# Performance work log

Measured on AMD Instinct MI355X. Metric: run time of the kernel, lower is better.

Reference implementation:

```python
import jax, jax.numpy as jnp
import numpy as np

# spconv.SparseConv4d(C_in, 16, (1,3,3,3), stride=1, padding=0) on spatial_shape [1000,1000,40]:
# leading kernel dim is size 1, so this is a regular (non-submanifold) 3D sparse conv,
# valid padding -> output spatial shape (998, 998, 38). Implemented as gather-GEMM-scatter:
# input point p contributes feat(p) @ W[k] to output coord p - offset[k] for each of 27 taps.

N = 200000
C_IN = 64
C_OUT = 16
K = 3
OUT_SP = (998, 998, 38)  # 1000-3+1, 1000-3+1, 40-3+1
SENT = OUT_SP[0] * OUT_SP[1] * OUT_SP[2]  # sentinel linear index for invalid taps


def setup_inputs() -> dict:
    key = jax.random.key(0)
    k1, k2, k3, k4, k5, k6 = jax.random.split(key, 6)
    feats = jax.random.normal(k1, (N, C_IN), dtype=jnp.float32)
    x = jax.random.randint(k2, (N,), 0, 1000, dtype=jnp.int32)
    y = jax.random.randint(k3, (N,), 0, 1000, dtype=jnp.int32)
    z = jax.random.randint(k4, (N,), 0, 40, dtype=jnp.int32)
    coords = jnp.stack([jnp.zeros((N,), jnp.int32), x, y, z], axis=1)  # [N,4] (b,x,y,z)
    fan_in = C_IN * K * K * K
    W = jax.random.normal(k5, (K * K * K, C_IN, C_OUT), dtype=jnp.float32) / np.sqrt(fan_in)
    bias = jax.random.normal(k6, (C_OUT,), dtype=jnp.float32) * 0.01
    return {"input": feats, "coords": coords, "W": W, "bias": bias}


def reference(input, coords, W, bias):
    # kernel tap offsets, C-order over (kx,ky,kz) in [0,3)^3 -> [27,3]
    off = jnp.stack(
        jnp.meshgrid(jnp.arange(K), jnp.arange(K), jnp.arange(K), indexing="ij"),
        axis=-1,
    ).reshape(K * K * K, 3).astype(jnp.int32)
    xyz = coords[:, 1:4]                              # [N,3]
    oc = xyz[:, None, :] - off[None, :, :]            # [N,27,3] output coord per tap
    out_sp = jnp.array(OUT_SP, dtype=jnp.int32)
    valid = jnp.all((oc >= 0) & (oc < out_sp), axis=-1)  # [N,27]
    lin = oc[..., 0] * (OUT_SP[1] * OUT_SP[2]) + oc[..., 1] * OUT_SP[2] + oc[..., 2]
    lin = jnp.where(valid, lin, SENT).reshape(-1)     # [N*27]

    # gather-GEMM: per-tap GEMM over all active voxels
    contrib = jnp.einsum("nc,kco->nko", input, W)     # [N,27,16]
    contrib = jnp.where(valid[..., None], contrib, 0.0).reshape(-1, C_OUT)

    NK = N * (K * K * K)
    uniq, inv = jnp.unique(lin, return_inverse=True, size=NK, fill_value=SENT)
    inv = inv.reshape(-1)
    # scatter-add into unique output sites
    out = jax.ops.segment_sum(contrib, inv, num_segments=NK)  # [NK,16]
    cnt = jax.ops.segment_sum(valid.reshape(-1).astype(jnp.int32), inv, num_segments=NK)
    out = out + jnp.where(cnt[:, None] > 0, bias[None, :], 0.0)
    return out, uniq
```

## Files before the change

kernel.cpp:

```cpp
#include <hip/hip_runtime.h>

#define N_PTS   200000
#define CIN     64
#define COUT    16
#define KK      27
#define SXD     998
#define SYD     998
#define SZD     38
#define STRX    (SYD*SZD)
#define SENTV   (SXD*SYD*SZD)
#define NKTOT   (N_PTS*KK)
#define NWORDS  ((SENTV+31)/32)
#define NCHUNK  ((NWORDS+255)/256)

typedef float f32x4 __attribute__((ext_vector_type(4)));

__global__ void mark_kernel(const int* __restrict__ coords, unsigned* __restrict__ bitmap,
                            unsigned* __restrict__ multi) {
    int n = blockIdx.x * blockDim.x + threadIdx.x;
    if (n >= N_PTS) return;
    int4 c = ((const int4*)coords)[n];
    int x = c.y, y = c.z, z = c.w;
    int zlo = z - 2; if (zlo < 0) zlo = 0;
    int zhi = z;     if (zhi > SZD - 1) zhi = SZD - 1;
    unsigned nb = (unsigned)(zhi - zlo + 1);
    unsigned mseed = (1u << nb) - 1u;
    #pragma unroll
    for (int dx = 0; dx < 3; dx++) {
        int ox = x - dx;
        if (ox < 0 || ox >= SXD) continue;
        #pragma unroll
        for (int dy = 0; dy < 3; dy++) {
            int oy = y - dy;
            if (oy < 0 || oy >= SYD) continue;
            int lin = ox*STRX + oy*SZD + zlo;
            unsigned w = (unsigned)lin >> 5;
            unsigned b = (unsigned)lin & 31u;
            unsigned lowm = mseed << b;
            unsigned old = atomicOr(&bitmap[w], lowm);
            unsigned col = old & lowm;
            if (col) atomicOr(&multi[w], col);
            if (b + nb > 32u) {
                unsigned highm = mseed >> (32u - b);
                unsigned old2 = atomicOr(&bitmap[w+1], highm);
                unsigned col2 = old2 & highm;
                if (col2) atomicOr(&multi[w+1], col2);
            }
        }
    }
}

__global__ void chunk_sums_kernel(const unsigned* __restrict__ bitmap, unsigned* __restrict__ csums) {
    int w = blockIdx.x * 256 + threadIdx.x;
    unsigned c = (w < NWORDS) ? (unsigned)__popc(bitmap[w]) : 0u;
    __shared__ unsigned s[256];
    s[threadIdx.x] = c;
    __syncthreads();
    for (int off = 128; off > 0; off >>= 1) {
        if (threadIdx.x < off) s[threadIdx.x] += s[threadIdx.x + off];
        __syncthreads();
    }
    if (threadIdx.x == 0) csums[blockIdx.x] = s[0];
}

__global__ void scan_chunks_kernel(const unsigned* __restrict__ csums,
                                   unsigned* __restrict__ cprefix,
                                   unsigned* __restrict__ Uptr) {
    __shared__ unsigned s[256];
    __shared__ unsigned run_s;
    if (threadIdx.x == 0) run_s = 0;
    __syncthreads();
    for (int base = 0; base < NCHUNK; base += 256) {
        int i = base + threadIdx.x;
        unsigned v = (i < NCHUNK) ? csums[i] : 0u;
        s[threadIdx.x] = v;
        __syncthreads();
        for (int off = 1; off < 256; off <<= 1) {
            unsigned t = (threadIdx.x >= off) ? s[threadIdx.x - off] : 0u;
            __syncthreads();
            s[threadIdx.x] += t;
            __syncthreads();
        }
        unsigned run = run_s;
        if (i < NCHUNK) cprefix[i] = run + s[threadIdx.x] - v;
        unsigned tile_total = s[255];
        __syncthreads();
        if (threadIdx.x == 255) run_s = run + tile_total;
        __syncthreads();
    }
    if (threadIdx.x == 0) Uptr[0] = run_s;
}

__global__ void word_prefix_kernel(const unsigned* __restrict__ bitmap,
                                   const unsigned* __restrict__ cprefix,
                                   unsigned* __restrict__ wprefix) {
    int w = blockIdx.x * 256 + threadIdx.x;
    unsigned v = (w < NWORDS) ? (unsigned)__popc(bitmap[w]) : 0u;
    __shared__ unsigned s[256];
    s[threadIdx.x] = v;
    __syncthreads();
    for (int off = 1; off < 256; off <<= 1) {
        unsigned t = (threadIdx.x >= off) ? s[threadIdx.x - off] : 0u;
        __syncthreads();
        s[threadIdx.x] += t;
        __syncthreads();
    }
    if (w < NWORDS) wprefix[w] = cprefix[blockIdx.x] + s[threadIdx.x] - v;
}

__global__ void fill_out_kernel(float* __restrict__ out, const float* __restrict__ bias,
                                const unsigned* __restrict__ Uptr) {
    unsigned U = Uptr[0];
    unsigned i = blockIdx.x * blockDim.x + threadIdx.x;
    if (i >= (unsigned)NKTOT * 4u) return;
    unsigned row = i >> 2;
    int q = i & 3;
    float4 v;
    if (row < U) v = ((const float4*)bias)[q];
    else         v = make_float4(0.f, 0.f, 0.f, 0.f);
    ((float4*)out)[i] = v;
}

__global__ void fill_uniq_kernel(float* __restrict__ uniq) {
    unsigned i = blockIdx.x * blockDim.x + threadIdx.x;
    if (i < (unsigned)NKTOT) uniq[i] = (float)SENTV;
}

__global__ void tail_kernel(float* __restrict__ out, float* __restrict__ uniq,
                            const unsigned* __restrict__ Uptr) {
    unsigned U = Uptr[0];
    unsigned i = blockIdx.x * blockDim.x + threadIdx.x;
    if (i >= (unsigned)NKTOT || i < U) return;
    f32x4 z4 = {0.f, 0.f, 0.f, 0.f};
    f32x4* dst = (f32x4*)(out + (size_t)i * COUT);
    #pragma unroll
    for (int q = 0; q < 4; q++) __builtin_nontemporal_store(z4, dst + q);
    __builtin_nontemporal_store((float)SENTV, uniq + i);
}

__global__ void write_uniq_kernel(const unsigned* __restrict__ bitmap,
                                  const unsigned* __restrict__ multi,
                                  const unsigned* __restrict__ wprefix,
                                  float* __restrict__ uniq,
                                  float* __restrict__ out,
                                  const float* __restrict__ bias,
                                  int do_bias) {
    int w = blockIdx.x * 256 + threadIdx.x;
    if (w >= NWORDS) return;
    unsigned bits = bitmap[w];
    if (!bits) return;
    unsigned mbits = do_bias ? multi[w] : 0u;
    f32x4 bv[4];
    #pragma unroll
    for (int q = 0; q < 4; q++) bv[q] = ((const f32x4*)bias)[q];
    unsigned r = wprefix[w];
    while (bits) {
        int b = __ffs(bits) - 1;
        bits &= bits - 1;
        uniq[r] = (float)(w * 32 + b);
        if ((mbits >> b) & 1u) {
            f32x4* dst = (f32x4*)(out + (size_t)r * COUT);
            #pragma unroll
            for (int q = 0; q < 4; q++) __builtin_nontemporal_store(bv[q], dst + q);
        }
        r++;
    }
}

__launch_bounds__(64)
__global__ void scatter_mm_kernel(const float* __restrict__ feats,
                                  const int* __restrict__ coords,
                                  const float* __restrict__ W,
                                  const float* __restrict__ bias,
                                  const unsigned* __restrict__ bitmap,
                                  const unsigned* __restrict__ multi,
                                  const unsigned* __restrict__ wprefix,
                                  float* __restrict__ out) {
    int n = blockIdx.x * 64 + threadIdx.x;
    if (n >= N_PTS) return;
    int4 cc = ((const int4*)coords)[n];
    int x = cc.y, y = cc.z, z = cc.w;

    f32x4 f[CIN/4];
    const f32x4* fin4 = (const f32x4*)(feats + (size_t)n * CIN);
    #pragma unroll
    for (int i = 0; i < CIN/4; i++) f[i] = __builtin_nontemporal_load(fin4 + i);

    f32x4 bv[4];
    #pragma unroll
    for (int q = 0; q < 4; q++) bv[q] = ((const f32x4*)bias)[q];

    #pragma unroll 1
    for (int m = 0; m < KK; m++) {
        int ox = x - (m/9), oy = y - ((m/3)%3), oz = z - (m%3);
        if (ox < 0 || ox >= SXD || oy < 0 || oy >= SYD || oz < 0 || oz >= SZD) continue;
        int lin = ox*STRX + oy*SZD + oz;
        unsigned word = (unsigned)lin >> 5, bit = (unsigned)lin & 31u;
        unsigned rank = wprefix[word] + (unsigned)__popc(bitmap[word] & ((1u << bit) - 1u));
        bool is_multi = (multi[word] >> bit) & 1u;

        const float* wk = W + (size_t)m * CIN * COUT;
        float acc[COUT];
        #pragma unroll
        for (int o = 0; o < COUT; o++) acc[o] = 0.f;
        #pragma unroll
        for (int c4 = 0; c4 < CIN/4; c4++) {
            f32x4 fv = f[c4];
            const float* wrow = wk + c4 * 4 * COUT;
            #pragma unroll
            for (int o = 0; o < COUT; o++) {
                acc[o] += fv.x * wrow[o] + fv.y * wrow[COUT + o]
                        + fv.z * wrow[2*COUT + o] + fv.w * wrow[3*COUT + o];
            }
        }

        float* dst = out + (size_t)rank * COUT;
        if (!is_multi) {
            #pragma unroll
            for (int q = 0; q < 4; q++) {
                f32x4 v;
                v.x = acc[q*4+0] + bv[q].x;
                v.y = acc[q*4+1] + bv[q].y;
                v.z = acc[q*4+2] + bv[q].z;
                v.w = acc[q*4+3] + bv[q].w;
                __builtin_nontemporal_store(v, ((f32x4*)dst) + q);
            }
        } else {
            #pragma unroll
            for (int o = 0; o < COUT; o++) atomicAdd(dst + o, acc[o]);
        }
    }
}

extern "C" void kernel_launch(void* const* d_in, const int* in_sizes, int n_in,
                              void* d_out, int out_size, void* d_ws, size_t ws_size,
                              hipStream_t stream) {
    const float* feats  = (const float*)d_in[0];
    const int*   coords = (const int*)d_in[1];
    const float* W      = (const float*)d_in[2];
    const float* bias   = (const float*)d_in[3];
    float* out  = (float*)d_out;
    float* uniq = out + (size_t)NKTOT * COUT;

    unsigned* ws      = (unsigned*)d_ws;
    unsigned* bitmap  = ws;
    unsigned* multi   = ws + NWORDS;
    unsigned* wprefix = ws + 2 * (size_t)NWORDS;
    unsigned* csums   = ws + 3 * (size_t)NWORDS;
    unsigned* cprefix = csums + NCHUNK;
    unsigned* Uptr    = cprefix + NCHUNK;

    size_t needed = ((size_t)3 * NWORDS + 2 * NCHUNK + 1) * sizeof(unsigned);
    bool have_multi = ws_size >= needed;
    if (!have_multi) {
        multi   = bitmap;
        wprefix = ws + NWORDS;
        csums   = ws + 2 * (size_t)NWORDS;
        cprefix = csums + NCHUNK;
        Uptr    = cprefix + NCHUNK;
        hipMemsetAsync(bitmap, 0, (size_t)NWORDS * sizeof(unsigned), stream);
    } else {
        hipMemsetAsync(bitmap, 0, 2 * (size_t)NWORDS * sizeof(unsigned), stream);
    }

    mark_kernel<<<(N_PTS + 255) / 256, 256, 0, stream>>>(coords, bitmap, multi);
    chunk_sums_kernel<<<NCHUNK, 256, 0, stream>>>(bitmap, csums);
    scan_chunks_kernel<<<1, 256, 0, stream>>>(csums, cprefix, Uptr);
    word_prefix_kernel<<<NCHUNK, 256, 0, stream>>>(bitmap, cprefix, wprefix);

    if (have_multi) {
        write_uniq_kernel<<<NCHUNK, 256, 0, stream>>>(bitmap, multi, wprefix, uniq, out, bias, 1);
        tail_kernel<<<(NKTOT + 255) / 256, 256, 0, stream>>>(out, uniq, Uptr);
    } else {
        fill_out_kernel<<<(NKTOT * 4 + 255) / 256, 256, 0, stream>>>(out, bias, Uptr);
        fill_uniq_kernel<<<(NKTOT + 255) / 256, 256, 0, stream>>>(uniq);
        write_uniq_kernel<<<NCHUNK, 256, 0, stream>>>(bitmap, multi, wprefix, uniq, out, bias, 0);
    }

    scatter_mm_kernel<<<(N_PTS + 63) / 64, 64, 0, stream>>>(
        feats, coords, W, bias, bitmap, multi, wprefix, out);
}
```

Baseline: 1.253 ms.

## Interleave bitmap metadata, bucket-sort points spatially, and stage uniq writes in LDS

Bitmap, multi-mask and word prefix are interleaved into one 16-byte record per word, so the scatter kernel needs a single uint4 load per tap instead of three scattered loads. Points are bucket-sorted by coarse (x/8, y/8) tiles using a histogram, an exclusive scan and an atomic placement pass. Neighbouring threads therefore touch nearby bitmap words and output rows. write_uniq now gathers each block's unique indices in shared memory and writes them out coalesced, in exchange for extra passes, more workspace and an 8192-float shared buffer per block.

```diff
diff --git a/kernel.cpp b/kernel.cpp
--- a/kernel.cpp
+++ b/kernel.cpp
@@ -12,15 +12,21 @@
 #define NKTOT   (N_PTS*KK)
 #define NWORDS  ((SENTV+31)/32)
 #define NCHUNK  ((NWORDS+255)/256)
+#define NB      16000
 
 typedef float f32x4 __attribute__((ext_vector_type(4)));
 
-__global__ void mark_kernel(const int* __restrict__ coords, unsigned* __restrict__ bitmap,
-                            unsigned* __restrict__ multi) {
+template<int S>
+__global__ void mark_kernel(const int* __restrict__ coords, unsigned* __restrict__ bm,
+                            unsigned* __restrict__ mu, unsigned* __restrict__ hist) {
     int n = blockIdx.x * blockDim.x + threadIdx.x;
     if (n >= N_PTS) return;
     int4 c = ((const int4*)coords)[n];
     int x = c.y, y = c.z, z = c.w;
+    if (hist) {
+        unsigned key = ((unsigned)x >> 3) * 128u + ((unsigned)y >> 3);
+        atomicAdd(&hist[key], 1u);
+    }
     int zlo = z - 2; if (zlo < 0) zlo = 0;
     int zhi = z;     if (zhi > SZD - 1) zhi = SZD - 1;
     unsigned nb = (unsigned)(zhi - zlo + 1);
@@ -37,22 +43,23 @@
             unsigned w = (unsigned)lin >> 5;
             unsigned b = (unsigned)lin & 31u;
             unsigned lowm = mseed << b;
-            unsigned old = atomicOr(&bitmap[w], lowm);
+            unsigned old = atomicOr(&bm[(size_t)w * S], lowm);
             unsigned col = old & lowm;
-            if (col) atomicOr(&multi[w], col);
+            if (col) atomicOr(&mu[(size_t)w * S], col);
             if (b + nb > 32u) {
                 unsigned highm = mseed >> (32u - b);
-                unsigned old2 = atomicOr(&bitmap[w+1], highm);
+                unsigned old2 = atomicOr(&bm[(size_t)(w+1) * S], highm);
                 unsigned col2 = old2 & highm;
-                if (col2) atomicOr(&multi[w+1], col2);
+                if (col2) atomicOr(&mu[(size_t)(w+1) * S], col2);
             }
         }
     }
 }
 
-__global__ void chunk_sums_kernel(const unsigned* __restrict__ bitmap, unsigned* __restrict__ csums) {
+template<int S>
+__global__ void chunk_sums_kernel(const unsigned* __restrict__ bm, unsigned* __restrict__ csums) {
     int w = blockIdx.x * 256 + threadIdx.x;
-    unsigned c = (w < NWORDS) ? (unsigned)__popc(bitmap[w]) : 0u;
+    unsigned c = (w < NWORDS) ? (unsigned)__popc(bm[(size_t)w * S]) : 0u;
     __shared__ unsigned s[256];
     s[threadIdx.x] = c;
     __syncthreads();
@@ -63,9 +70,12 @@
     if (threadIdx.x == 0) csums[blockIdx.x] = s[0];
 }
 
-__global__ void scan_chunks_kernel(const unsigned* __restrict__ csums,
-                                   unsigned* __restrict__ cprefix,
-                                   unsigned* __restrict__ Uptr) {
+__global__ void scan_all_kernel(const unsigned* __restrict__ csums,
+                                unsigned* __restrict__ cprefix,
+                                unsigned* __restrict__ Uptr,
+                                const unsigned* __restrict__ hist,
+                                unsigned* __restrict__ bpos,
+                                int do_buckets) {
     __shared__ unsigned s[256];
     __shared__ unsigned run_s;
     if (threadIdx.x == 0) run_s = 0;
@@ -89,13 +99,36 @@
         __syncthreads();
     }
     if (threadIdx.x == 0) Uptr[0] = run_s;
-}
-
-__global__ void word_prefix_kernel(const unsigned* __restrict__ bitmap,
+    if (!do_buckets) return;
+    __syncthreads();
+    if (threadIdx.x == 0) run_s = 0;
+    __syncthreads();
+    for (int base = 0; base < NB; base += 256) {
+        int i = base + threadIdx.x;
+        unsigned v = (i < NB) ? hist[i] : 0u;
+        s[threadIdx.x] = v;
+        __syncthreads();
+        for (int off = 1; off < 256; off <<= 1) {
+            unsigned t = (threadIdx.x >= off) ? s[threadIdx.x - off] : 0u;
+            __syncthreads();
+            s[threadIdx.x] += t;
+            __syncthreads();
+        }
+        unsigned run = run_s;
+        if (i < NB) bpos[i] = run + s[threadIdx.x] - v;
+        unsigned tile_total = s[255];
+        __syncthreads();
+        if (threadIdx.x == 255) run_s = run + tile_total;
+        __syncthreads();
+    }
+}
+
+template<int S>
+__global__ void word_prefix_kernel(const unsigned* __restrict__ bm,
                                    const unsigned* __restrict__ cprefix,
-                                   unsigned* __restrict__ wprefix) {
+                                   unsigned* __restrict__ wp) {
     int w = blockIdx.x * 256 + threadIdx.x;
-    unsigned v = (w < NWORDS) ? (unsigned)__popc(bitmap[w]) : 0u;
+    unsigned v = (w < NWORDS) ? (unsigned)__popc(bm[(size_t)w * S]) : 0u;
     __shared__ unsigned s[256];
     s[threadIdx.x] = v;
     __syncthreads();
@@ -105,7 +138,17 @@
         s[threadIdx.x] += t;
         __syncthreads();
     }
-    if (w < NWORDS) wprefix[w] = cprefix[blockIdx.x] + s[threadIdx.x] - v;
+    if (w < NWORDS) wp[(size_t)w * S] = cprefix[blockIdx.x] + s[threadIdx.x] - v;
+}
+
+__global__ void pidx_kernel(const int* __restrict__ coords, unsigned* __restrict__ bpos,
+                            int4* __restrict__ csorted) {
+    int n = blockIdx.x * blockDim.x + threadIdx.x;
+    if (n >= N_PTS) return;
+    int4 c = ((const int4*)coords)[n];
+    unsigned key = ((unsigned)c.y >> 3) * 128u + ((unsigned)c.z >> 3);
+    unsigned pos = atomicAdd(&bpos[key], 1u);
+    csorted[pos] = make_int4(n, c.y, c.z, c.w);
 }
 
 __global__ void fill_out_kernel(float* __restrict__ out, const float* __restrict__ bias,
@@ -138,53 +181,76 @@
     __builtin_nontemporal_store((float)SENTV, uniq + i);
 }
 
-__global__ void write_uniq_kernel(const unsigned* __restrict__ bitmap,
-                                  const unsigned* __restrict__ multi,
-                                  const unsigned* __restrict__ wprefix,
+template<int S, bool DO_BIAS>
+__global__ void write_uniq_kernel(const unsigned* __restrict__ bm,
+                                  const unsigned* __restrict__ mu,
+                                  const unsigned* __restrict__ wp,
+                                  const unsigned* __restrict__ Uptr,
                                   float* __restrict__ uniq,
                                   float* __restrict__ out,
-                                  const float* __restrict__ bias,
-                                  int do_bias) {
-    int w = blockIdx.x * 256 + threadIdx.x;
-    if (w >= NWORDS) return;
-    unsigned bits = bitmap[w];
-    if (!bits) return;
-    unsigned mbits = do_bias ? multi[w] : 0u;
-    f32x4 bv[4];
-    #pragma unroll
-    for (int q = 0; q < 4; q++) bv[q] = ((const f32x4*)bias)[q];
-    unsigned r = wprefix[w];
-    while (bits) {
-        int b = __ffs(bits) - 1;
-        bits &= bits - 1;
-        uniq[r] = (float)(w * 32 + b);
-        if ((mbits >> b) & 1u) {
-            f32x4* dst = (f32x4*)(out + (size_t)r * COUT);
-            #pragma unroll
-            for (int q = 0; q < 4; q++) __builtin_nontemporal_store(bv[q], dst + q);
-        }
-        r++;
-    }
-}
-
+                                  const float* __restrict__ bias) {
+    __shared__ float sbuf[8192];
+    unsigned U = Uptr[0];
+    int wfirst = blockIdx.x * 256;
+    int wnext  = wfirst + 256;
+    unsigned r0 = wp[(size_t)wfirst * S];
+    unsigned r1 = (wnext < NWORDS) ? wp[(size_t)wnext * S] : U;
+    int w = wfirst + threadIdx.x;
+    unsigned bits = 0, r = 0, mbits = 0;
+    if (w < NWORDS) {
+        bits = bm[(size_t)w * S];
+        r    = wp[(size_t)w * S];
+        if (DO_BIAS) mbits = mu[(size_t)w * S];
+    }
+    unsigned bb = bits, rr = r;
+    while (bb) {
+        int b = __ffs(bb) - 1;
+        bb &= bb - 1;
+        sbuf[rr - r0] = (float)((unsigned)w * 32u + b);
+        rr++;
+    }
+    __syncthreads();
+    unsigned span = r1 - r0;
+    for (unsigned j = threadIdx.x; j < span; j += 256)
+        __builtin_nontemporal_store(sbuf[j], uniq + r0 + j);
+    if (DO_BIAS && bits && mbits) {
+        f32x4 bv[4];
+        #pragma unroll
+        for (int q = 0; q < 4; q++) bv[q] = ((const f32x4*)bias)[q];
+        bb = bits; rr = r;
+        while (bb) {
+            int b = __ffs(bb) - 1;
+            bb &= bb - 1;
+            if ((mbits >> b) & 1u) {
+                f32x4* dst = (f32x4*)(out + (size_t)rr * COUT);
+                #pragma unroll
+                for (int q = 0; q < 4; q++) __builtin_nontemporal_store(bv[q], dst + q);
+            }
+            rr++;
+        }
+    }
+}
+
+template<int S, bool SORTED>
 __launch_bounds__(64)
 __global__ void scatter_mm_kernel(const float* __restrict__ feats,
-                                  const int* __restrict__ coords,
+                                  const int4* __restrict__ cpts,
                                   const float* __restrict__ W,
                                   const float* __restrict__ bias,
-                                  const unsigned* __restrict__ bitmap,
-                                  const unsigned* __restrict__ multi,
-                                  const unsigned* __restrict__ wprefix,
+                                  const unsigned* __restrict__ bm,
+                                  const unsigned* __restrict__ mu,
+                                  const unsigned* __restrict__ wp,
                                   float* __restrict__ out) {
-    int n = blockIdx.x * 64 + threadIdx.x;
-    if (n >= N_PTS) return;
-    int4 cc = ((const int4*)coords)[n];
+    int i = blockIdx.x * 64 + threadIdx.x;
+    if (i >= N_PTS) return;
+    int4 cc = cpts[i];
+    int n = SORTED ? cc.x : i;
     int x = cc.y, y = cc.z, z = cc.w;
 
     f32x4 f[CIN/4];
     const f32x4* fin4 = (const f32x4*)(feats + (size_t)n * CIN);
     #pragma unroll
-    for (int i = 0; i < CIN/4; i++) f[i] = __builtin_nontemporal_load(fin4 + i);
+    for (int q = 0; q < CIN/4; q++) f[q] = __builtin_nontemporal_load(fin4 + q);
 
     f32x4 bv[4];
     #pragma unroll
@@ -196,8 +262,16 @@
         if (ox < 0 || ox >= SXD || oy < 0 || oy >= SYD || oz < 0 || oz >= SZD) continue;
         int lin = ox*STRX + oy*SZD + oz;
         unsigned word = (unsigned)lin >> 5, bit = (unsigned)lin & 31u;
-        unsigned rank = wprefix[word] + (unsigned)__popc(bitmap[word] & ((1u << bit) - 1u));
-        bool is_multi = (multi[word] >> bit) & 1u;
+        unsigned rank;
+        bool is_multi;
+        if constexpr (S == 4) {
+            uint4 md = ((const uint4*)bm)[word];
+            rank = md.z + (unsigned)__popc(md.x & ((1u << bit) - 1u));
+            is_multi = (md.y >> bit) & 1u;
+        } else {
+            rank = wp[word] + (unsigned)__popc(bm[word] & ((1u << bit) - 1u));
+            is_multi = (mu[word] >> bit) & 1u;
+        }
 
         const float* wk = W + (size_t)m * CIN * COUT;
         float acc[COUT];
@@ -242,41 +316,54 @@
     float* out  = (float*)d_out;
     float* uniq = out + (size_t)NKTOT * COUT;
 
-    unsigned* ws      = (unsigned*)d_ws;
-    unsigned* bitmap  = ws;
-    unsigned* multi   = ws + NWORDS;
-    unsigned* wprefix = ws + 2 * (size_t)NWORDS;
-    unsigned* csums   = ws + 3 * (size_t)NWORDS;
-    unsigned* cprefix = csums + NCHUNK;
-    unsigned* Uptr    = cprefix + NCHUNK;
-
-    size_t needed = ((size_t)3 * NWORDS + 2 * NCHUNK + 1) * sizeof(unsigned);
-    bool have_multi = ws_size >= needed;
-    if (!have_multi) {
-        multi   = bitmap;
-        wprefix = ws + NWORDS;
-        csums   = ws + 2 * (size_t)NWORDS;
-        cprefix = csums + NCHUNK;
-        Uptr    = cprefix + NCHUNK;
+    unsigned* ws = (unsigned*)d_ws;
+
+    size_t o_meta    = 0;
+    size_t o_hist    = o_meta + 4 * (size_t)NWORDS;
+    size_t o_bpos    = o_hist + NB;
+    size_t o_csums   = o_bpos + NB;
+    size_t o_cprefix = o_csums + NCHUNK;
+    size_t o_Uptr    = o_cprefix + NCHUNK;
+    size_t o_csort   = (o_Uptr + 1 + 3) & ~(size_t)3;
+    size_t fast_words = o_csort + 4 * (size_t)N_PTS;
+
+    if (ws_size >= fast_words * sizeof(unsigned)) {
+        unsigned* meta    = ws + o_meta;
+        unsigned* hist    = ws + o_hist;
+        unsigned* bpos    = ws + o_bpos;
+        unsigned* csums   = ws + o_csums;
+        unsigned* cprefix = ws + o_cprefix;
+        unsigned* Uptr    = ws + o_Uptr;
+        int4*     csorted = (int4*)(ws + o_csort);
+
+        hipMemsetAsync(meta, 0, (4 * (size_t)NWORDS + NB) * sizeof(unsigned), stream);
+        mark_kernel<4><<<(N_PTS + 255) / 256, 256, 0, stream>>>(coords, meta, meta + 1, hist);
+        chunk_sums_kernel<4><<<NCHUNK, 256, 0, stream>>>(meta, csums);
+        scan_all_kernel<<<1, 256, 0, stream>>>(csums, cprefix, Uptr, hist, bpos, 1);
+        pidx_kernel<<<(N_PTS + 255) / 256, 256, 0, stream>>>(coords, bpos, csorted);
+        word_prefix_kernel<4><<<NCHUNK, 256, 0, stream>>>(meta, cprefix, meta + 2);
+        write_uniq_kernel<4, true><<<NCHUNK, 256, 0, stream>>>(
+            meta, meta + 1, meta + 2, Uptr, uniq, out, bias);
+        tail_kernel<<<(NKTOT + 255) / 256, 256, 0, stream>>>(out, uniq, Uptr);
+        scatter_mm_kernel<4, true><<<(N_PTS + 63) / 64, 64, 0, stream>>>(
+            feats, csorted, W, bias, meta, meta + 1, meta + 2, out);
+    } else {
+        unsigned* bitmap  = ws;
+        unsigned* wprefix = ws + NWORDS;
+        unsigned* csums   = ws + 2 * (size_t)NWORDS;
+        unsigned* cprefix = csums + NCHUNK;
+        unsigned* Uptr    = cprefix + NCHUNK;
+
         hipMemsetAsync(bitmap, 0, (size_t)NWORDS * sizeof(unsigned), stream);
-    } else {
-        hipMemsetAsync(bitmap, 0, 2 * (size_t)NWORDS * sizeof(unsigned), stream);
-    }
-
-    mark_kernel<<<(N_PTS + 255) / 256, 256, 0, stream>>>(coords, bitmap, multi);
-    chunk_sums_kernel<<<NCHUNK, 256, 0, stream>>>(bitmap, csums);
-    scan_chunks_kernel<<<1, 256, 0, stream>>>(csums, cprefix, Uptr);
-    word_prefix_kernel<<<NCHUNK, 256, 0, stream>>>(bitmap, cprefix, wprefix);
-
-    if (have_multi) {
-        write_uniq_kernel<<<NCHUNK, 256, 0, stream>>>(bitmap, multi, wprefix, uniq, out, bias, 1);
-        tail_kernel<<<(NKTOT + 255) / 256, 256, 0, stream>>>(out, uniq, Uptr);
-    } else {
+        mark_kernel<1><<<(N_PTS + 255) / 256, 256, 0, stream>>>(coords, bitmap, bitmap, nullptr);
+        chunk_sums_kernel<1><<<NCHUNK, 256, 0, stream>>>(bitmap, csums);
+        scan_all_kernel<<<1, 256, 0, stream>>>(csums, cprefix, Uptr, nullptr, nullptr, 0);
+        word_prefix_kernel<1><<<NCHUNK, 256, 0, stream>>>(bitmap, cprefix, wprefix);
         fill_out_kernel<<<(NKTOT * 4 + 255) / 256, 256, 0, stream>>>(out, bias, Uptr);
         fill_uniq_kernel<<<(NKTOT + 255) / 256, 256, 0, stream>>>(uniq);
-        write_uniq_kernel<<<NCHUNK, 256, 0, stream>>>(bitmap, multi, wprefix, uniq, out, bias, 0);
-    }
-
-    scatter_mm_kernel<<<(N_PTS + 63) / 64, 64, 0, stream>>>(
-        feats, coords, W, bias, bitmap, multi, wprefix, out);
-}
+        write_uniq_kernel<1, false><<<NCHUNK, 256, 0, stream>>>(
+            bitmap, bitmap, wprefix, Uptr, uniq, out, bias);
+        scatter_mm_kernel<1, false><<<(N_PTS + 63) / 64, 64, 0, stream>>>(
+            feats, (const int4*)coords, W, bias, bitmap, bitmap, wprefix, out);
+    }
+}
```

Result: slower. 1.300 ms (+3.7%).
